# Optimization experiments

Hardware: AMD Instinct MI355X
Metric: run time of the kernel (lower is better)

The kernel has to match this reference:

```python
import jax, jax.numpy as jnp
import numpy as np

B, T, F, H = 8, 1024, 256, 256
EPS = 1e-5


def layer_norm(x, w, b):
    m = jnp.mean(x, axis=-1, keepdims=True)
    v = jnp.var(x, axis=-1, keepdims=True)
    return (x - m) / jnp.sqrt(v + EPS) * w + b


def setup_inputs() -> dict:
    key = jax.random.key(0)
    ks = jax.random.split(key, 8)
    x = jax.random.normal(ks[0], (B, T, F, 2), dtype=jnp.float32)
    # 8 attention branches, each with its own q/k/v Linear(F -> H).
    # Stored as [8, F, H] (already transposed vs torch's [out,in]).
    Wq = jax.random.normal(ks[1], (8, F, H), dtype=jnp.float32) * 0.02
    Wk = jax.random.normal(ks[2], (8, F, H), dtype=jnp.float32) * 0.02
    Wv = jax.random.normal(ks[3], (8, F, H), dtype=jnp.float32) * 0.02
    bq = jax.random.normal(ks[4], (8, H), dtype=jnp.float32) * 0.02
    bk = jax.random.normal(ks[5], (8, H), dtype=jnp.float32) * 0.02
    bv = jax.random.normal(ks[6], (8, H), dtype=jnp.float32) * 0.02
    ln1_w = jnp.ones((F,), jnp.float32)
    ln1_b = jnp.zeros((F,), jnp.float32)
    ln2_w = jnp.ones((H,), jnp.float32)
    ln2_b = jnp.zeros((H,), jnp.float32)
    return {"x": x, "Wq": Wq, "bq": bq, "Wk": Wk, "bk": bk, "Wv": Wv,
            "bv": bv, "ln1_w": ln1_w, "ln1_b": ln1_b,
            "ln2_w": ln2_w, "ln2_b": ln2_b}


def reference(x, Wq, bq, Wk, bk, Wv, bv, ln1_w, ln1_b, ln2_w, ln2_b):
    # LayerNorm over the in_channel (frequency) axis, per real/imag plane
    xn = jnp.swapaxes(layer_norm(jnp.swapaxes(x, 2, 3), ln1_w, ln1_b), 2, 3)
    real, imag = xn[..., 0], xn[..., 1]  # each [B,T,F]
    # branch order: A(r,r,r) B(r,i,i) C(i,r,i) D(i,i,r) E(r,r,i) F(r,i,r) G(i,r,r) H(i,i,i)
    qs = jnp.stack([real, real, imag, imag, real, real, imag, imag])  # [8,B,T,F]
    ks_ = jnp.stack([real, imag, real, imag, real, imag, real, imag])
    vs = jnp.stack([real, imag, imag, real, imag, real, real, imag])
    q = jnp.einsum('nbtf,nfh->nbth', qs, Wq) + bq[:, None, None, :]
    k = jnp.einsum('nbtf,nfh->nbth', ks_, Wk) + bk[:, None, None, :]
    v = jnp.einsum('nbtf,nfh->nbth', vs, Wv) + bv[:, None, None, :]
    scale = 1.0 / (Wq.shape[-1] ** 0.5)
    energy = jnp.einsum('nbth,nbsh->nbts', q, k) * scale  # [8,B,T,T]
    attn = jax.nn.softmax(energy, axis=-1)
    o = jnp.einsum('nbts,nbsh->nbth', attn, v)  # [8,B,T,H]
    real_att = o[0] - o[1] - o[2] - o[3]
    imag_att = o[4] + o[5] + o[6] - o[7]
    out = jnp.stack([real_att, imag_att], axis=-1)  # [B,T,H,2]
    out = jnp.swapaxes(layer_norm(jnp.swapaxes(out, 2, 3), ln2_w, ln2_b), 2, 3)
    return out
```

## Files before the change

### kernel.cpp

```cpp
#include <hip/hip_runtime.h>
#include <math.h>

#define B_ 8
#define T_ 1024
#define F_ 256
#define H_ 256
#define BT_ (B_*T_)
constexpr float EPS = 1e-5f;
constexpr float SCALE_L2E = 0.09016844005555963f;

typedef unsigned int u32;
typedef unsigned short u16;
typedef __attribute__((ext_vector_type(8))) short bf16x8;
typedef __attribute__((ext_vector_type(4))) float f32x4;
typedef __attribute__((ext_vector_type(16))) float f32x16;

__device__ __forceinline__ float bf1(u16 p) { return __uint_as_float(((u32)p) << 16); }
__device__ __forceinline__ u16 f2bf(float f) {
  u32 u = __float_as_uint(f);
  u32 r = u + 0x7FFFu + ((u >> 16) & 1u);
  return (u16)(r >> 16);
}

__device__ __forceinline__ f32x4 mfma16(bf16x8 a, bf16x8 b, f32x4 c) {
  return __builtin_amdgcn_mfma_f32_16x16x32_bf16(a, b, c, 0, 0, 0);
}
__device__ __forceinline__ f32x16 mfma32(bf16x8 a, bf16x8 b, f32x16 c) {
  return __builtin_amdgcn_mfma_f32_32x32x16_bf16(a, b, c, 0, 0, 0);
}

__device__ __forceinline__ void gload_lds16(const u16* g, u16* l) {
  __builtin_amdgcn_global_load_lds(
      (const __attribute__((address_space(1))) u32*)(uintptr_t)g,
      (__attribute__((address_space(3))) u32*)(u32)(uintptr_t)l,
      16, 0, 0);
}

__device__ __forceinline__ void block_reduce4(float& a, float& b, float& c, float& d) {
  #pragma unroll
  for (int off = 32; off > 0; off >>= 1) {
    a += __shfl_down(a, off, 64);
    b += __shfl_down(b, off, 64);
    c += __shfl_down(c, off, 64);
    d += __shfl_down(d, off, 64);
  }
  __shared__ float red[4][4];
  int wid = threadIdx.x >> 6;
  int lane = threadIdx.x & 63;
  if (lane == 0) { red[0][wid] = a; red[1][wid] = b; red[2][wid] = c; red[3][wid] = d; }
  __syncthreads();
  a = red[0][0] + red[0][1] + red[0][2] + red[0][3];
  b = red[1][0] + red[1][1] + red[1][2] + red[1][3];
  c = red[2][0] + red[2][1] + red[2][2] + red[2][3];
  d = red[3][0] + red[3][1] + red[3][2] + red[3][3];
}

__global__ __launch_bounds__(256) void prep_kernel(
    const float* __restrict__ x, const float* __restrict__ w, const float* __restrict__ bi,
    u16* __restrict__ xnr, u16* __restrict__ xni,
    const float* __restrict__ Wq, const float* __restrict__ Wk, const float* __restrict__ Wv,
    u16* __restrict__ wT) {
  const int tid = threadIdx.x;
  if (blockIdx.x < BT_) {
    const int row = blockIdx.x;
    const int f = tid;
    float2 xv = reinterpret_cast<const float2*>(x)[row * F_ + f];
    float sr = xv.x, si = xv.y, sr2 = xv.x * xv.x, si2 = xv.y * xv.y;
    block_reduce4(sr, si, sr2, si2);
    const float inv = 1.0f / F_;
    float mr = sr * inv, mi = si * inv;
    float vr = sr2 * inv - mr * mr, vi = si2 * inv - mi * mi;
    float rr = rsqrtf(vr + EPS), ri = rsqrtf(vi + EPS);
    float ww = w[f], bb = bi[f];
    xnr[row * F_ + f] = f2bf((xv.x - mr) * rr * ww + bb);
    xni[row * F_ + f] = f2bf((xv.y - mi) * ri * ww + bb);
  } else {
    const int wid = blockIdx.x - BT_;
    const int z = wid >> 4;
    const int r4 = wid & 15;
    const int ft = (r4 & 3) * 64;
    const int ht = (r4 >> 2) * 64;
    const int m = z >> 3, n = z & 7;
    const float* W = (m == 0 ? Wq : (m == 1 ? Wk : Wv)) + (size_t)n * F_ * H_;
    __shared__ __align__(16) u16 Ts[64][72];

    #pragma unroll
    for (int i = 0; i < 4; i++) {
      int id = tid + i * 256;
      int r = id >> 4, c4 = (id & 15) * 4;
      float4 p = *reinterpret_cast<const float4*>(&W[(size_t)(ft + r) * H_ + ht + c4]);
      Ts[r][c4 + 0] = f2bf(p.x); Ts[r][c4 + 1] = f2bf(p.y);
      Ts[r][c4 + 2] = f2bf(p.z); Ts[r][c4 + 3] = f2bf(p.w);
    }
    __syncthreads();
    u16* op = wT + (size_t)z * F_ * H_ + (size_t)ht * F_ + ft;
    #pragma unroll
    for (int i = 0; i < 2; i++) {
      int id = tid + i * 256;
      int hl = id & 63, g = id >> 6;
      u16 tmp[8];
      #pragma unroll
      for (int j = 0; j < 8; j++) tmp[j] = Ts[g * 8 + j][hl];
      *reinterpret_cast<uint4*>(op + (size_t)hl * F_ + g * 8) =
          *reinterpret_cast<const uint4*>(tmp);
    }
  }
}

__global__ __launch_bounds__(256, 2) void qkv_kernel(
    const u16* __restrict__ xnr, const u16* __restrict__ xni, const u16* __restrict__ wT,
    const float* __restrict__ bq, const float* __restrict__ bk, const float* __restrict__ bv,
    u16* __restrict__ qo, u16* __restrict__ ko, u16* __restrict__ vTo) {
  const int z = blockIdx.y;
  const int m = z >> 3, n = z & 7;
  int sel; const float* bias; u16* out;
  if (m == 0)      { sel = (n >> 1) & 1;  bias = bq; out = qo + (size_t)n * BT_ * H_; }
  else if (m == 1) { sel = n & 1;         bias = bk; out = ko + (size_t)n * BT_ * H_; }
  else             { sel = __popc(n) & 1; bias = bv; out = nullptr; }
  const float osc = (m == 0) ? SCALE_L2E : 1.0f;
  const u16* A = sel ? xni : xnr;
  const u16* wp = wT + (size_t)z * F_ * H_;
  bias += n * H_;
  const int rowbase = blockIdx.x * 128;

  __shared__ __align__(16) u16 As[2][128 * 32];
  __shared__ __align__(16) u16 Bs[2][256 * 32];
  __shared__ __align__(16) u16 Epi[4][1536];

  const int tid = threadIdx.x;
  const int wv = tid >> 6, lane = tid & 63;
  const int quad = lane >> 4, l16 = lane & 15;
  const int wrow = wv >> 1, wcol = wv & 1;

  f32x4 acc[4][8];
  #pragma unroll
  for (int i = 0; i < 4; i++)
    #pragma unroll
    for (int j = 0; j < 8; j++) acc[i][j] = (f32x4){0.f, 0.f, 0.f, 0.f};

  const int ar = tid >> 2;
  const int ak = (tid & 3) * 8;

  #pragma unroll 1
  for (int kb = 0; kb < F_; kb += 64) {
    #pragma unroll
    for (int h = 0; h < 2; h++) {
      gload_lds16(A + (size_t)(rowbase + ar) * F_ + kb + h * 32 + ak,
                  &As[h][tid * 8]);
      gload_lds16(A + (size_t)(rowbase + 64 + ar) * F_ + kb + h * 32 + ak,
                  &As[h][2048 + tid * 8]);
      #pragma unroll
      for (int c = 0; c < 4; c++)
        gload_lds16(wp + (size_t)(c * 64 + ar) * F_ + kb + h * 32 + ak,
                    &Bs[h][c * 2048 + tid * 8]);
    }
    __syncthreads();
    #pragma unroll
    for (int h = 0; h < 2; h++) {
      bf16x8 a[4], b[8];
      #pragma unroll
      for (int mi = 0; mi < 4; mi++)
        a[mi] = *reinterpret_cast<const bf16x8*>(
            &As[h][(wrow * 64 + mi * 16 + l16) * 32 + quad * 8]);
      #pragma unroll
      for (int nj = 0; nj < 8; nj++)
        b[nj] = *reinterpret_cast<const bf16x8*>(
            &Bs[h][(wcol * 128 + nj * 16 + l16) * 32 + quad * 8]);
      #pragma unroll
      for (int mi = 0; mi < 4; mi++)
        #pragma unroll
        for (int nj = 0; nj < 8; nj++)
          acc[mi][nj] = mfma16(a[mi], b[nj], acc[mi][nj]);
    }
    __syncthreads();
  }

  float bias8[8];
  #pragma unroll
  for (int nj = 0; nj < 8; nj++)
    bias8[nj] = bias[wcol * 128 + nj * 16 + l16];

  if (m != 2) {
    #pragma unroll
    for (int pass = 0; pass < 2; pass++) {
      #pragma unroll
      for (int mi = 0; mi < 4; mi++) {
        #pragma unroll
        for (int nj4 = 0; nj4 < 4; nj4++) {
          int nj = pass * 4 + nj4;
          #pragma unroll
          for (int r = 0; r < 4; r++)
            Epi[wv][(quad * 4 + r) * 72 + nj4 * 16 + l16] =
                f2bf((acc[mi][nj][r] + bias8[nj]) * osc);
        }
        int row = rowbase + wrow * 64 + mi * 16 + l16;
        uint4 v0 = *reinterpret_cast<const uint4*>(&Epi[wv][l16 * 72 + quad * 16]);
        uint4 v1 = *reinterpret_cast<const uint4*>(&Epi[wv][l16 * 72 + quad * 16 + 8]);
        u16* op = out + (size_t)row * H_ + wcol * 128 + pass * 64 + quad * 16;
        *reinterpret_cast<uint4*>(op) = v0;
        *reinterpret_cast<uint4*>(op + 8) = v1;
      }
    }
  } else {
    #pragma unroll
    for (int pass = 0; pass < 2; pass++) {
      #pragma unroll
      for (int mi = 0; mi < 4; mi++) {
        #pragma unroll
        for (int nj4 = 0; nj4 < 4; nj4++) {
          int nj = pass * 4 + nj4;
          #pragma unroll
          for (int r = 0; r < 4; r++)
            Epi[wv][(nj4 * 16 + l16) * 24 + quad * 4 + r] =
                f2bf(acc[mi][nj][r] + bias8[nj]);
        }
        int hloc = lane;
        uint4 w0 = *reinterpret_cast<const uint4*>(&Epi[wv][hloc * 24]);
        uint4 w1 = *reinterpret_cast<const uint4*>(&Epi[wv][hloc * 24 + 8]);
        u16* op = vTo + (size_t)n * H_ * BT_ +
                  (size_t)(wcol * 128 + pass * 64 + hloc) * BT_ +
                  rowbase + wrow * 64 + mi * 16;
        *reinterpret_cast<uint4*>(op) = w0;
        *reinterpret_cast<uint4*>(op + 8) = w1;
      }
    }
  }
}

__global__ __launch_bounds__(512, 2) void attn_kernel(
    const u16* __restrict__ q, const u16* __restrict__ k, const u16* __restrict__ vT,
    u16* __restrict__ obuf) {
  const int fid = blockIdx.x;
  const int qt = fid >> 6;
  const int nb = fid & 63;
  const int n = nb >> 3, b = nb & 7;
  const int tid = threadIdx.x;
  const int wv = tid >> 6, lane = tid & 63;
  const int hi = lane >> 5, l32 = lane & 31;
  const int qh = wv >> 1;
  const int kh = wv & 1;
  const int hh = wv & 1;

  const size_t base = (size_t)nb * T_ * H_;
  const u16* qp = q + base;
  const u16* kp = k + base;
  const u16* vtp = vT + ((size_t)n * H_ * B_ + b) * T_;

  __shared__ __align__(16) u16 Ks[2][64][256];
  __shared__ __align__(16) u16 Vs[2][64][256];
  __shared__ __align__(16) u16 Ps[4][32][72];

  const int qrow0 = qt * 128 + qh * 32;
  bf16x8 qf[16];
  #pragma unroll
  for (int kc = 0; kc < 16; kc++)
    qf[kc] = *reinterpret_cast<const bf16x8*>(
        qp + (size_t)(qrow0 + l32) * H_ + kc * 16 + hi * 8);

  f32x16 o[4];
  #pragma unroll
  for (int ot = 0; ot < 4; ot++)
    #pragma unroll
    for (int r = 0; r < 16; r++) o[ot][r] = 0.f;
  float lper[16];
  #pragma unroll
  for (int r = 0; r < 16; r++) lper[r] = 0.f;

  auto stage_k = [&](int ktN, int buf) {
    #pragma unroll
    for (int i = 0; i < 4; i++) {
      int idx = wv * 4 + i;
      int row = 2 * idx + hi;
      const u16* src = kp + (size_t)(ktN * 64 + row) * H_ +
                       ((l32 ^ (row & 31)) * 8);
      gload_lds16(src, &Ks[buf][2 * idx][0]);
    }
  };
  auto stage_v = [&](int ktN, int buf) {
    #pragma unroll
    for (int i = 0; i < 4; i++) {
      int idx = wv * 4 + i;
      int p = 2 * idx + hi;
      int u = l32 ^ (p & 7);
      const u16* src = vtp + (size_t)(p * 4 + (u >> 3)) * BT_ +
                       ktN * 64 + (u & 7) * 8;
      gload_lds16(src, &Vs[buf][2 * idx][0]);
    }
  };

  stage_k(0, 0); stage_v(0, 0);
  stage_k(1, 1); stage_v(1, 1);
  asm volatile("s_waitcnt vmcnt(8)" ::: "memory");
  __builtin_amdgcn_s_barrier();
  __builtin_amdgcn_sched_barrier(0);

  const int krow = kh * 32 + l32;

  #pragma unroll 1
  for (int kt = 0; kt < 16; kt++) {
    const int c = kt & 1;

    f32x16 sa, sb;
    #pragma unroll
    for (int r = 0; r < 16; r++) { sa[r] = 0.f; sb[r] = 0.f; }
    __builtin_amdgcn_s_setprio(1);
    #pragma unroll
    for (int kc = 0; kc < 16; kc += 2) {
      bf16x8 kfa = *reinterpret_cast<const bf16x8*>(
          &Ks[c][krow][(((kc * 2 + hi) ^ l32) * 8)]);
      bf16x8 kfb = *reinterpret_cast<const bf16x8*>(
          &Ks[c][krow][(((kc * 2 + 2 + hi) ^ l32) * 8)]);
      sa = mfma32(qf[kc], kfa, sa);
      sb = mfma32(qf[kc + 1], kfb, sb);
    }
    __builtin_amdgcn_s_setprio(0);

    #pragma unroll
    for (int r = 0; r < 16; r++) {
      float p = __builtin_amdgcn_exp2f(sa[r] + sb[r]);
      lper[r] += p;
      Ps[qh][(r & 3) + 8 * (r >> 2) + 4 * hi][kh * 32 + l32] = f2bf(p);
    }

    asm volatile("s_waitcnt lgkmcnt(0)" ::: "memory");
    __builtin_amdgcn_s_barrier();
    __builtin_amdgcn_sched_barrier(0);

    if (kt < 14) stage_k(kt + 2, c);

    bf16x8 pa[4];
    #pragma unroll
    for (int kc2 = 0; kc2 < 4; kc2++)
      pa[kc2] = *reinterpret_cast<const bf16x8*>(
          &Ps[qh][l32][kc2 * 16 + hi * 8]);
    __builtin_amdgcn_s_setprio(1);
    #pragma unroll
    for (int ot = 0; ot < 4; ot++) {
      const int p = hh * 32 + ot * 8 + (l32 >> 2);
      #pragma unroll
      for (int kc2 = 0; kc2 < 4; kc2++) {
        int s = ((l32 & 3) * 8 + kc2 * 2 + hi) ^ (l32 >> 2);
        bf16x8 vf = *reinterpret_cast<const bf16x8*>(&Vs[c][p][s * 8]);
        o[ot] = mfma32(pa[kc2], vf, o[ot]);
      }
    }
    __builtin_amdgcn_s_setprio(0);

    if (kt < 14) {
      asm volatile("s_waitcnt vmcnt(4)" ::: "memory");
    } else {
      asm volatile("s_waitcnt vmcnt(0)" ::: "memory");
    }
    __builtin_amdgcn_s_barrier();
    __builtin_amdgcn_sched_barrier(0);

    if (kt < 14) stage_v(kt + 2, c);
  }

  #pragma unroll
  for (int r = 0; r < 16; r++) {
    #pragma unroll
    for (int off = 1; off < 32; off <<= 1)
      lper[r] += __shfl_xor(lper[r], off, 64);
  }
  if (l32 == 0) {
    #pragma unroll
    for (int r = 0; r < 16; r++) {
      int row = (r & 3) + 8 * (r >> 2) + 4 * hi;
      *reinterpret_cast<float*>(&Ps[qh][row][64 + 2 * kh]) = lper[r];
    }
  }
  __syncthreads();

  float invl[16];
  #pragma unroll
  for (int r = 0; r < 16; r++) {
    int row = (r & 3) + 8 * (r >> 2) + 4 * hi;
    float l0 = *reinterpret_cast<const float*>(&Ps[qh][row][64]);
    float l1 = *reinterpret_cast<const float*>(&Ps[qh][row][66]);
    invl[r] = 1.0f / (l0 + l1);
  }

  u16* Ew = reinterpret_cast<u16*>(&Ks[0][0][0]) + wv * 1280;
  const int grow = b * 1024 + qrow0 + l32;
  #pragma unroll
  for (int ot = 0; ot < 4; ot++) {
    #pragma unroll
    for (int r = 0; r < 16; r++) {
      int row = (r & 3) + 8 * (r >> 2) + 4 * hi;
      Ew[row * 40 + l32] = f2bf(o[ot][r] * invl[r]);
    }
    int ht = hh * 4 + ot;
    uint4 v0 = *reinterpret_cast<const uint4*>(&Ew[l32 * 40 + hi * 16]);
    uint4 v1 = *reinterpret_cast<const uint4*>(&Ew[l32 * 40 + hi * 16 + 8]);
    u16* op = obuf + (((size_t)n * 8 + ht) * BT_ + grow) * 32 + hi * 16;
    *reinterpret_cast<uint4*>(op) = v0;
    *reinterpret_cast<uint4*>(op + 8) = v1;
  }
}

__global__ __launch_bounds__(256) void combine_ln2_kernel(
    const u16* __restrict__ obuf, const float* __restrict__ w,
    const float* __restrict__ bi, float* __restrict__ out) {
  const int row = blockIdx.x;
  const int h = threadIdx.x;
  float o[8];
  #pragma unroll
  for (int nn = 0; nn < 8; nn++)
    o[nn] = bf1(obuf[(((size_t)nn * 8 + (h >> 5)) * BT_ + row) * 32 + (h & 31)]);
  float re = o[0] - o[1] - o[2] - o[3];
  float im = o[4] + o[5] + o[6] - o[7];
  float sr = re, si = im, sr2 = re * re, si2 = im * im;
  block_reduce4(sr, si, sr2, si2);
  const float inv = 1.0f / H_;
  float mr = sr * inv, mi = si * inv;
  float vr = sr2 * inv - mr * mr, vi = si2 * inv - mi * mi;
  float rr = rsqrtf(vr + EPS), ri = rsqrtf(vi + EPS);
  float ww = w[h], bb = bi[h];
  float2 res;
  res.x = (re - mr) * rr * ww + bb;
  res.y = (im - mi) * ri * ww + bb;
  reinterpret_cast<float2*>(out)[(size_t)row * H_ + h] = res;
}

extern "C" void kernel_launch(void* const* d_in, const int* in_sizes, int n_in,
                              void* d_out, int out_size, void* d_ws, size_t ws_size,
                              hipStream_t stream) {
  const float* x    = (const float*)d_in[0];
  const float* Wq   = (const float*)d_in[1];
  const float* bq   = (const float*)d_in[2];
  const float* Wk   = (const float*)d_in[3];
  const float* bk   = (const float*)d_in[4];
  const float* Wv   = (const float*)d_in[5];
  const float* bv   = (const float*)d_in[6];
  const float* ln1w = (const float*)d_in[7];
  const float* ln1b = (const float*)d_in[8];
  const float* ln2w = (const float*)d_in[9];
  const float* ln2b = (const float*)d_in[10];

  char* ws = (char*)d_ws;
  u16* xnr  = (u16*)(ws);
  u16* xni  = (u16*)(ws + (4ull  << 20));
  u16* wTb  = (u16*)(ws + (8ull  << 20));
  u16* obuf = (u16*)(ws);
  u16* vT   = (u16*)(ws + (32ull << 20));
  u16* qbuf = (u16*)(ws + (64ull << 20));
  u16* kbuf = (u16*)(ws + (96ull << 20));

  prep_kernel<<<BT_ + 384, 256, 0, stream>>>(x, ln1w, ln1b, xnr, xni,
                                             Wq, Wk, Wv, wTb);
  qkv_kernel<<<dim3(64, 24), 256, 0, stream>>>(xnr, xni, wTb, bq, bk, bv,
                                               qbuf, kbuf, vT);
  attn_kernel<<<dim3(512), 512, 0, stream>>>(qbuf, kbuf, vT, obuf);
  combine_ln2_kernel<<<BT_, 256, 0, stream>>>(obuf, ln2w, ln2b, (float*)d_out);
}
```

Measured before the change: 167.0 us.

## Double-buffer QKV projection K-loop with async LDS prefetch and manual waitcnt

Restructures the projection GEMM K-loop into 32-wide stages with two LDS buffers. The next-but-one stage's global-to-LDS loads are issued while the current stage's MFMAs run, and partial vmcnt waits replace full __syncthreads. It also raises wave priority around the MFMA block. The aim is to hide global load latency behind compute in this stage of the kernel. In exchange it relies on hand-written waitcnt counts (6 loads per stage), which must match the number of loads issued per stage to stay correct.

```diff
diff --git a/kernel.cpp b/kernel.cpp
--- a/kernel.cpp
+++ b/kernel.cpp
@@ -141,38 +141,57 @@
   const int ar = tid >> 2;
   const int ak = (tid & 3) * 8;
 
+  auto stage = [&](int t, int buf) {
+    const int kb = t * 32;
+    gload_lds16(A + (size_t)(rowbase + ar) * F_ + kb + ak, &As[buf][tid * 8]);
+    gload_lds16(A + (size_t)(rowbase + 64 + ar) * F_ + kb + ak,
+                &As[buf][2048 + tid * 8]);
+    #pragma unroll
+    for (int c = 0; c < 4; c++)
+      gload_lds16(wp + (size_t)(c * 64 + ar) * F_ + kb + ak,
+                  &Bs[buf][c * 2048 + tid * 8]);
+  };
+
+  stage(0, 0);
+  stage(1, 1);
+  asm volatile("s_waitcnt vmcnt(6)" ::: "memory");
+  __builtin_amdgcn_s_barrier();
+  __builtin_amdgcn_sched_barrier(0);
+
   #pragma unroll 1
-  for (int kb = 0; kb < F_; kb += 64) {
-    #pragma unroll
-    for (int h = 0; h < 2; h++) {
-      gload_lds16(A + (size_t)(rowbase + ar) * F_ + kb + h * 32 + ak,
-                  &As[h][tid * 8]);
-      gload_lds16(A + (size_t)(rowbase + 64 + ar) * F_ + kb + h * 32 + ak,
-                  &As[h][2048 + tid * 8]);
-      #pragma unroll
-      for (int c = 0; c < 4; c++)
-        gload_lds16(wp + (size_t)(c * 64 + ar) * F_ + kb + h * 32 + ak,
-                    &Bs[h][c * 2048 + tid * 8]);
-    }
-    __syncthreads();
-    #pragma unroll
-    for (int h = 0; h < 2; h++) {
-      bf16x8 a[4], b[8];
-      #pragma unroll
-      for (int mi = 0; mi < 4; mi++)
-        a[mi] = *reinterpret_cast<const bf16x8*>(
-            &As[h][(wrow * 64 + mi * 16 + l16) * 32 + quad * 8]);
+  for (int t = 0; t < 8; t++) {
+    const int c = t & 1;
+
+    bf16x8 a[4], b[8];
+    #pragma unroll
+    for (int mi = 0; mi < 4; mi++)
+      a[mi] = *reinterpret_cast<const bf16x8*>(
+          &As[c][(wrow * 64 + mi * 16 + l16) * 32 + quad * 8]);
+    #pragma unroll
+    for (int nj = 0; nj < 8; nj++)
+      b[nj] = *reinterpret_cast<const bf16x8*>(
+          &Bs[c][(wcol * 128 + nj * 16 + l16) * 32 + quad * 8]);
+    __builtin_amdgcn_s_setprio(1);
+    #pragma unroll
+    for (int mi = 0; mi < 4; mi++)
       #pragma unroll
       for (int nj = 0; nj < 8; nj++)
-        b[nj] = *reinterpret_cast<const bf16x8*>(
-            &Bs[h][(wcol * 128 + nj * 16 + l16) * 32 + quad * 8]);
-      #pragma unroll
-      for (int mi = 0; mi < 4; mi++)
-        #pragma unroll
-        for (int nj = 0; nj < 8; nj++)
-          acc[mi][nj] = mfma16(a[mi], b[nj], acc[mi][nj]);
-    }
-    __syncthreads();
+        acc[mi][nj] = mfma16(a[mi], b[nj], acc[mi][nj]);
+    __builtin_amdgcn_s_setprio(0);
+
+    asm volatile("s_waitcnt lgkmcnt(0)" ::: "memory");
+    __builtin_amdgcn_s_barrier();
+    __builtin_amdgcn_sched_barrier(0);
+
+    if (t < 6) stage(t + 2, c);
+
+    if (t < 6) {
+      asm volatile("s_waitcnt vmcnt(6)" ::: "memory");
+    } else {
+      asm volatile("s_waitcnt vmcnt(0)" ::: "memory");
+    }
+    __builtin_amdgcn_s_barrier();
+    __builtin_amdgcn_sched_barrier(0);
   }
 
   float bias8[8];
```

After: 165.8 us (median of 2 runs). About the same (-0.7%).
